# Optimization experiments

Measured on AMD Instinct MI355X. Metric: run time of the kernel, lower is better.

Reference implementation:

```python
import jax, jax.numpy as jnp
import numpy as np

TOPK, NUM_CLASSES, ALPHA, BETA, EPS = 13, 80, 1.0, 6.0, 1e-9
IOU_EPS = 1e-7  # eps used inside bbox_iou (ultralytics default)


def ciou(box1, box2):
    # box1, box2: broadcastable [..., 4] in xyxy format; returns CIoU [..., 1]
    b1x1, b1y1, b1x2, b1y2 = jnp.split(box1, 4, axis=-1)
    b2x1, b2y1, b2x2, b2y2 = jnp.split(box2, 4, axis=-1)
    w1, h1 = b1x2 - b1x1, b1y2 - b1y1 + IOU_EPS
    w2, h2 = b2x2 - b2x1, b2y2 - b2y1 + IOU_EPS
    inter = (jnp.clip(jnp.minimum(b1x2, b2x2) - jnp.maximum(b1x1, b2x1), 0.0) *
             jnp.clip(jnp.minimum(b1y2, b2y2) - jnp.maximum(b1y1, b2y1), 0.0))
    union = w1 * h1 + w2 * h2 - inter + IOU_EPS
    iou = inter / union
    cw = jnp.maximum(b1x2, b2x2) - jnp.minimum(b1x1, b2x1)  # enclosing box width
    ch = jnp.maximum(b1y2, b2y2) - jnp.minimum(b1y1, b2y1)
    c2 = cw ** 2 + ch ** 2 + IOU_EPS
    rho2 = ((b2x1 + b2x2 - b1x1 - b1x2) ** 2 + (b2y1 + b2y2 - b1y1 - b1y2) ** 2) / 4.0
    v = (4.0 / np.pi ** 2) * (jnp.arctan(w2 / h2) - jnp.arctan(w1 / h1)) ** 2
    alpha = jax.lax.stop_gradient(v / (v - iou + (1.0 + IOU_EPS)))  # torch: with no_grad
    return iou - (rho2 / c2 + v * alpha)


def tal_forward(pd_scores, pd_bboxes, anc_points, gt_labels, gt_bboxes, mask_gt):
    bs, na, nc = pd_scores.shape
    nb = gt_bboxes.shape[1]
    dt = pd_scores.dtype
    mgt = mask_gt[..., 0]  # (b, nb)

    # --- select_candidates_in_gts: anchor center strictly inside gt box ---
    lt, rb = gt_bboxes[..., :2], gt_bboxes[..., 2:]
    deltas = jnp.concatenate([anc_points[None, None, :, :] - lt[:, :, None, :],
                              rb[:, :, None, :] - anc_points[None, None, :, :]], axis=-1)  # (b,nb,na,4)
    mask_in_gts = (deltas.min(-1) > EPS).astype(dt)  # (b,nb,na)
    valid = (mask_in_gts * mgt[:, :, None]) > 0  # bool (b,nb,na)

    # --- get_box_metrics: class score gather + pairwise CIoU, masked ---
    lbl = gt_labels[..., 0].astype(jnp.int32)  # (b,nb)
    scores = jnp.take_along_axis(pd_scores, lbl[:, None, :], axis=2)  # (b,na,nb)
    bbox_scores = jnp.where(valid, scores.transpose(0, 2, 1), 0.0)  # (b,nb,na)
    ov = ciou(gt_bboxes[:, :, None, :], pd_bboxes[:, None, :, :])[..., 0]  # (b,nb,na)
    overlaps = jnp.where(valid, jnp.clip(ov, 0.0), 0.0)
    align_metric = bbox_scores ** ALPHA * overlaps ** BETA

    # --- select_topk_candidates ---
    _, tk_i = jax.lax.top_k(align_metric, TOPK)  # (b,nb,TOPK)
    tk_i = jnp.where(mgt[:, :, None] > 0, tk_i, 0)  # invalid gt rows -> all idx 0 (counted >1 -> zeroed)
    flat_i = tk_i.reshape(bs * nb, TOPK)
    cnt = jnp.zeros((bs * nb, na), jnp.int32).at[jnp.arange(bs * nb)[:, None], flat_i].add(1)
    cnt = cnt.reshape(bs, nb, na)
    is_in_topk = jnp.where(cnt > 1, 0, cnt).astype(dt)
    mask_pos = is_in_topk * mask_in_gts * mgt[:, :, None]

    # --- select_highest_overlaps: resolve anchors claimed by multiple gts ---
    fg = mask_pos.sum(-2)  # (b,na)
    mask_multi = fg[:, None, :] > 1
    max_idx = overlaps.argmax(1)  # (b,na)
    is_max = jax.nn.one_hot(max_idx, nb, dtype=dt).transpose(0, 2, 1)  # (b,nb,na)
    mask_pos = jnp.where(mask_multi, is_max, mask_pos)
    fg_mask = mask_pos.sum(-2)  # (b,na)
    target_gt_idx = mask_pos.argmax(-2)  # (b,na)

    # --- get_targets ---
    flat_gt_idx = target_gt_idx + jnp.arange(bs)[:, None] * nb  # (b,na)
    target_labels = jnp.clip(lbl.reshape(-1)[flat_gt_idx], 0)
    target_bboxes = gt_bboxes.reshape(-1, 4)[flat_gt_idx]  # (b,na,4)
    target_scores = jax.nn.one_hot(target_labels, nc, dtype=dt)
    target_scores = jnp.where(fg_mask[..., None] > 0, target_scores, 0.0)

    # --- normalization of align metric ---
    align_metric = align_metric * mask_pos
    pos_align = align_metric.max(-1, keepdims=True)  # (b,nb,1)
    pos_over = (overlaps * mask_pos).max(-1, keepdims=True)
    norm = (align_metric * pos_over / (pos_align + EPS)).max(-2)[..., None]  # (b,na,1)
    target_scores = target_scores * norm
    return target_labels, target_bboxes, target_scores, fg_mask > 0, target_gt_idx


def _make_boxes(key, shape):
    kc, kw = jax.random.split(key)
    c = jax.random.uniform(kc, shape[:-1] + (2,), jnp.float32, 60.0, 580.0)
    wh = jax.random.uniform(kw, shape[:-1] + (2,), jnp.float32, 20.0, 120.0)
    return jnp.concatenate([c - wh / 2, c + wh / 2], axis=-1)


def setup_inputs() -> dict:
    key = jax.random.key(0)
    ks = jax.random.split(key, 6)
    bs, na, nc, nb = 32, 8400, 80, 64
    pd_scores = jax.random.uniform(ks[0], (bs, na, nc), jnp.float32)
    pd_bboxes = _make_boxes(ks[1], (bs, na, 4))
    anc_points = jax.random.uniform(ks[2], (na, 2), jnp.float32, 0.0, 640.0)
    gt_labels = jax.random.randint(ks[3], (bs, nb, 1), 0, nc, dtype=jnp.int32)
    gt_bboxes = _make_boxes(ks[4], (bs, nb, 4))
    mask_gt = (jax.random.uniform(ks[5], (bs, nb, 1)) < 0.8).astype(jnp.float32)
    return {"pd_scores": pd_scores, "pd_bboxes": pd_bboxes, "anc_points": anc_points,
            "gt_labels": gt_labels, "gt_bboxes": gt_bboxes, "mask_gt": mask_gt}


def reference(pd_scores, pd_bboxes, anc_points, gt_labels, gt_bboxes, mask_gt):
    return tal_forward(pd_scores, pd_bboxes, anc_points, gt_labels, gt_bboxes, mask_gt)
```

## Files before the change

kernel.cpp:

```cpp
#include <hip/hip_runtime.h>
#include <stdint.h>

#pragma clang fp contract(off)

#define BS 32
#define NB 64
#define NA 8400
#define NC 80
#define TK 13
#define QMAX 1024
#define FORCED 32

__device__ __forceinline__ float ciou_f(float g0, float g1, float g2, float g3,
                                        float p0, float p1, float p2, float p3) {
    const float E = 1e-7f;
    float w1 = g2 - g0, h1 = (g3 - g1) + E;
    float w2 = p2 - p0, h2 = (p3 - p1) + E;
    float iw = fminf(g2, p2) - fmaxf(g0, p0); iw = fmaxf(iw, 0.f);
    float ih = fminf(g3, p3) - fmaxf(g1, p1); ih = fmaxf(ih, 0.f);
    float inter = iw * ih;
    float uni = w1 * h1 + w2 * h2 - inter + E;
    float iou = inter / uni;
    float cw = fmaxf(g2, p2) - fminf(g0, p0);
    float ch = fmaxf(g3, p3) - fminf(g1, p1);
    float c2 = cw * cw + ch * ch + E;
    float dx = p0 + p2 - g0 - g2;
    float dy = p1 + p3 - g1 - g3;
    float rho2 = (dx * dx + dy * dy) / 4.0f;
    float da = atanf(w2 / h2) - atanf(w1 / h1);
    float v = 0.4052847345693511f * (da * da);
    float alpha = v / ((v - iou) + 1.0000001f);
    return iou - (rho2 / c2 + v * alpha);
}

__global__ __launch_bounds__(256) void k1_topk(
    const float* __restrict__ pd_scores,
    const float* __restrict__ pd_bboxes,
    const float* __restrict__ anc,
    const int* __restrict__ gt_labels,
    const float* __restrict__ gt_bboxes,
    const float* __restrict__ mask_gt,
    int* __restrict__ tk_a, float* __restrict__ tk_v,
    float* __restrict__ tk_o, int* __restrict__ tk_f)
{
    int r = blockIdx.x;
    int b = r >> 6;
    int tid = threadIdx.x;

    if (mask_gt[r] <= 0.f) {
        if (tid < TK) {
            tk_a[r * TK + tid] = 0; tk_v[r * TK + tid] = 0.f;
            tk_o[r * TK + tid] = 0.f; tk_f[r * TK + tid] = 0;
        }
        return;
    }

    __shared__ int   qn;
    __shared__ int   qa[QMAX];
    __shared__ float qv[QMAX];
    __shared__ float qo[QMAX];

    float4 g = *(const float4*)&gt_bboxes[r * 4];
    int lbl = gt_labels[r];
    if (tid == 0) qn = 0;
    __syncthreads();

    for (int a = tid; a < NA; a += 256) {
        float2 ap = *(const float2*)&anc[2 * a];
        float d0 = ap.x - g.x, d1 = ap.y - g.y, d2 = g.z - ap.x, d3 = g.w - ap.y;
        float dmin = fminf(fminf(d0, d1), fminf(d2, d3));
        bool in = dmin > 1e-9f;
        if (in || a < FORCED) {
            int p = atomicAdd(&qn, 1);
            if (p < QMAX) qa[p] = a | (in ? (1 << 30) : 0);
        }
    }
    __syncthreads();
    int n = min(qn, QMAX);

    for (int c = tid; c < n; c += 256) {
        int packed = qa[c]; int a = packed & 0x3fffffff; bool in = (packed >> 30) & 1;
        float align = 0.f, ov = 0.f;
        if (in) {
            float4 p = *(const float4*)&pd_bboxes[(b * NA + a) * 4];
            ov = fmaxf(ciou_f(g.x, g.y, g.z, g.w, p.x, p.y, p.z, p.w), 0.f);
            float sc = pd_scores[(b * NA + a) * NC + lbl];
            float o2 = ov * ov;
            align = sc * (o2 * o2 * o2);
        }
        qv[c] = align; qo[c] = ov;
    }
    __syncthreads();

    if (tid < 64) {
        int lane = tid;
        unsigned consumed = 0;
        int wslot = 0; float wval = 0.f;
        for (int round = 0; round < TK; round++) {
            float bv = -2.f; int bgi = 0x7fffffff; int bsl = 0;
            int li = 0;
            for (int c = lane; c < n; c += 64, li++) {
                if (consumed & (1u << li)) continue;
                float v = qv[c]; int gi = qa[c] & 0x3fffffff;
                if (v > bv || (v == bv && gi < bgi)) { bv = v; bgi = gi; bsl = c; }
            }
            for (int off = 32; off; off >>= 1) {
                float v2 = __shfl_down(bv, off);
                int  gi2 = __shfl_down(bgi, off);
                int  sl2 = __shfl_down(bsl, off);
                if (v2 > bv || (v2 == bv && gi2 < bgi)) { bv = v2; bgi = gi2; bsl = sl2; }
            }
            int wsl = __shfl(bsl, 0);
            float wv = __shfl(bv, 0);
            if ((wsl & 63) == lane) consumed |= 1u << (wsl >> 6);
            if (lane == round) { wslot = wsl; wval = wv; }
        }
        if (lane < TK) {
            int packed = qa[wslot]; int a = packed & 0x3fffffff; int in = (packed >> 30) & 1;
            tk_a[r * TK + lane] = a;
            tk_v[r * TK + lane] = wval;
            tk_o[r * TK + lane] = qo[wslot];
            tk_f[r * TK + lane] = in;
        }
    }
}

__global__ void k2a_init(int* cnt, int* jA, unsigned* posA, unsigned* posO, int* mcount) {
    int i = blockIdx.x * 256 + threadIdx.x;
    if (i < BS * NA) { cnt[i] = 0; jA[i] = -1; }
    if (i < BS * NB) { posA[i] = 0u; posO[i] = 0u; }
    if (i == 0) *mcount = 0;
}

__global__ void k2b_count(const int* __restrict__ tk_a, const int* __restrict__ tk_f,
                          int* __restrict__ cnt) {
    int c = blockIdx.x * 256 + threadIdx.x;
    if (c >= BS * NB * TK) return;
    if (!tk_f[c]) return;
    int r = c / TK; int b = r >> 6;
    atomicAdd(&cnt[b * NA + tk_a[c]], 1);
}

__global__ void k2c_single(const int* __restrict__ tk_a, const float* __restrict__ tk_v,
                           const float* __restrict__ tk_o, const int* __restrict__ tk_f,
                           const int* __restrict__ cnt, int* __restrict__ jA,
                           float* __restrict__ av,
                           unsigned* __restrict__ posA, unsigned* __restrict__ posO,
                           int* __restrict__ mlist, int* __restrict__ mcount) {
    int c = blockIdx.x * 256 + threadIdx.x;
    if (c >= BS * NB * TK) return;
    if (!tk_f[c]) return;
    int r = c / TK; int b = r >> 6; int j = r & 63;
    int a = tk_a[c];
    int i = b * NA + a;
    if (cnt[i] == 1) {
        jA[i] = j; av[i] = tk_v[c];
        atomicMax(&posA[b * NB + j], __float_as_uint(tk_v[c]));
        atomicMax(&posO[b * NB + j], __float_as_uint(tk_o[c]));
    } else {
        int old = atomicCAS(&jA[i], -1, -2);
        if (old == -1) { int p = atomicAdd(mcount, 1); mlist[p] = i; }
    }
}

__global__ __launch_bounds__(256) void k2d_multi(
    const float* __restrict__ pd_scores,
    const float* __restrict__ pd_bboxes,
    const float* __restrict__ anc,
    const int* __restrict__ gt_labels,
    const float* __restrict__ gt_bboxes,
    const float* __restrict__ mask_gt,
    const int* __restrict__ mlist, const int* __restrict__ mcount,
    int* __restrict__ jA, float* __restrict__ av,
    unsigned* __restrict__ posA, unsigned* __restrict__ posO)
{
    int wid = (blockIdx.x * 256 + threadIdx.x) >> 6;
    int lane = threadIdx.x & 63;
    int nwaves = (gridDim.x * 256) >> 6;
    int nm = *mcount;
    for (int e = wid; e < nm; e += nwaves) {
        int i = mlist[e];
        int b = i / NA, a = i - b * NA;
        float2 ap = *(const float2*)&anc[2 * a];
        int row = b * NB + lane;
        float o = 0.f;
        if (mask_gt[row] > 0.f) {
            float4 g = *(const float4*)&gt_bboxes[row * 4];
            float d0 = ap.x - g.x, d1 = ap.y - g.y, d2 = g.z - ap.x, d3 = g.w - ap.y;
            float dmin = fminf(fminf(d0, d1), fminf(d2, d3));
            if (dmin > 1e-9f) {
                float4 p = *(const float4*)&pd_bboxes[(b * NA + a) * 4];
                o = fmaxf(ciou_f(g.x, g.y, g.z, g.w, p.x, p.y, p.z, p.w), 0.f);
            }
        }
        float bv = o; int bj = lane;
        for (int off = 32; off; off >>= 1) {
            float v2 = __shfl_down(bv, off);
            int  j2 = __shfl_down(bj, off);
            if (v2 > bv || (v2 == bv && j2 < bj)) { bv = v2; bj = j2; }
        }
        if (lane == 0) {
            int lbl = gt_labels[b * NB + bj];
            float sc = pd_scores[(b * NA + a) * NC + lbl];
            float o2 = bv * bv;
            float alg = sc * (o2 * o2 * o2);
            jA[i] = bj; av[i] = alg;
            atomicMax(&posA[b * NB + bj], __float_as_uint(alg));
            atomicMax(&posO[b * NB + bj], __float_as_uint(bv));
        }
    }
}

__global__ void k2f_final(const int* __restrict__ gt_labels,
                          const float* __restrict__ gt_bboxes,
                          const int* __restrict__ jA, const float* __restrict__ av,
                          const unsigned* __restrict__ posA, const unsigned* __restrict__ posO,
                          float* __restrict__ out,
                          float* __restrict__ normw, int* __restrict__ clsw) {
    int i = blockIdx.x * 256 + threadIdx.x;
    if (i >= BS * NA) return;
    int b = i / NA;
    int jj = jA[i];
    int tg = jj < 0 ? 0 : jj;
    int lab = gt_labels[b * NB + tg]; lab = lab < 0 ? 0 : lab;

    float* o_lab  = out;
    float* o_bbox = out + BS * NA;
    float* o_fg   = out + BS * NA * (5 + NC);
    float* o_idx  = o_fg + BS * NA;

    o_lab[i] = (float)lab;
    float4 bb = *(const float4*)&gt_bboxes[(b * NB + tg) * 4];
    *(float4*)&o_bbox[i * 4] = bb;
    o_fg[i] = (jj >= 0) ? 1.f : 0.f;
    o_idx[i] = (float)tg;

    float nrm = 0.f;
    if (jj >= 0) {
        float pa = __uint_as_float(posA[b * NB + jj]);
        float po = __uint_as_float(posO[b * NB + jj]);
        nrm = (av[i] * po) / (pa + 1e-9f);
    }
    normw[i] = nrm;
    clsw[i] = (jj >= 0) ? lab : -1;
}

__global__ void k3_scores(const float* __restrict__ normw, const int* __restrict__ clsw,
                          float* __restrict__ out) {
    int t = blockIdx.x * 256 + threadIdx.x;
    int row = t / 20;
    int c4 = (t - row * 20) * 4;
    int cls = clsw[row];
    float nv = normw[row];
    float4 v;
    v.x = (c4 + 0 == cls) ? nv : 0.f;
    v.y = (c4 + 1 == cls) ? nv : 0.f;
    v.z = (c4 + 2 == cls) ? nv : 0.f;
    v.w = (c4 + 3 == cls) ? nv : 0.f;
    float* o_sc = out + BS * NA * 5;
    *(float4*)&o_sc[row * NC + c4] = v;
}

extern "C" void kernel_launch(void* const* d_in, const int* in_sizes, int n_in,
                              void* d_out, int out_size, void* d_ws, size_t ws_size,
                              hipStream_t stream) {
    const float* pd_scores = (const float*)d_in[0];
    const float* pd_bboxes = (const float*)d_in[1];
    const float* anc       = (const float*)d_in[2];
    const int*   gt_labels = (const int*)d_in[3];
    const float* gt_bboxes = (const float*)d_in[4];
    const float* mask_gt   = (const float*)d_in[5];
    float* out = (float*)d_out;

    char* w = (char*)d_ws;
    const int NCAND = BS * NB * TK;
    int*      tk_a = (int*)w;      w += NCAND * 4;
    int*      tk_f = (int*)w;      w += NCAND * 4;
    float*    tk_v = (float*)w;    w += NCAND * 4;
    float*    tk_o = (float*)w;    w += NCAND * 4;
    int*      cnt  = (int*)w;      w += BS * NA * 4;
    int*      jA   = (int*)w;      w += BS * NA * 4;
    float*    av   = (float*)w;    w += BS * NA * 4;
    unsigned* posA = (unsigned*)w; w += BS * NB * 4;
    unsigned* posO = (unsigned*)w; w += BS * NB * 4;
    float*    normw = (float*)w;   w += BS * NA * 4;
    int*      clsw  = (int*)w;     w += BS * NA * 4;
    int*      mlist = (int*)w;     w += NCAND * 4;
    int*      mcount = (int*)w;    w += 4;

    k2a_init<<<(BS * NA + 255) / 256, 256, 0, stream>>>(cnt, jA, posA, posO, mcount);
    k1_topk<<<BS * NB, 256, 0, stream>>>(pd_scores, pd_bboxes, anc, gt_labels,
                                         gt_bboxes, mask_gt, tk_a, tk_v, tk_o, tk_f);
    k2b_count<<<(NCAND + 255) / 256, 256, 0, stream>>>(tk_a, tk_f, cnt);
    k2c_single<<<(NCAND + 255) / 256, 256, 0, stream>>>(tk_a, tk_v, tk_o, tk_f,
                                                        cnt, jA, av, posA, posO,
                                                        mlist, mcount);
    k2d_multi<<<52, 256, 0, stream>>>(pd_scores, pd_bboxes, anc, gt_labels,
                                      gt_bboxes, mask_gt, mlist, mcount,
                                      jA, av, posA, posO);
    k2f_final<<<(BS * NA + 255) / 256, 256, 0, stream>>>(gt_labels, gt_bboxes, jA, av,
                                                         posA, posO, out, normw, clsw);
    k3_scores<<<(BS * NA * NC / 4 + 255) / 256, 256, 0, stream>>>(normw, clsw, out);
}
```

Measured before the change: 223.5 us.

## Split candidate scan into separate anchor-parallel kernel and use single-wave top-k blocks

The in-box scan moves out of the per-GT top-k kernel into a new kernel where each thread takes one anchor, loops over the 64 GTs and appends matches to per-GT global lists through atomics. The top-k kernel then runs one 64-lane wave per GT, reads the precomputed list, adds the forced non-inside anchors with a ballot, and selects winners with less shared memory. The score output store becomes nontemporal. This adds one launch, global atomics and a workspace list capped at 640 entries per GT, and the order of list entries is no longer fixed, which only affects tie handling through anchor index.

```diff
diff --git a/kernel.cpp b/kernel.cpp
--- a/kernel.cpp
+++ b/kernel.cpp
@@ -8,8 +8,11 @@
 #define NA 8400
 #define NC 80
 #define TK 13
-#define QMAX 1024
+#define QCAP 640
+#define CMAX (QCAP + 32)
 #define FORCED 32
+
+typedef float floatx4 __attribute__((ext_vector_type(4)));
 
 __device__ __forceinline__ float ciou_f(float g0, float g1, float g2, float g3,
                                         float p0, float p1, float p2, float p3) {
@@ -33,102 +36,118 @@
     return iou - (rho2 / c2 + v * alpha);
 }
 
-__global__ __launch_bounds__(256) void k1_topk(
+__global__ __launch_bounds__(256) void k1a_scan(
+    const float* __restrict__ anc,
+    const float* __restrict__ gt_bboxes,
+    const float* __restrict__ mask_gt,
+    int* __restrict__ qcnt, int* __restrict__ qlist)
+{
+    int b = blockIdx.y;
+    int a = blockIdx.x * 256 + threadIdx.x;
+    if (a >= NA) return;
+    float2 ap = *(const float2*)&anc[2 * a];
+    for (int j = 0; j < NB; j++) {
+        int r = b * NB + j;
+        float mg = mask_gt[r];
+        float gx = gt_bboxes[r * 4 + 0], gy = gt_bboxes[r * 4 + 1];
+        float gz = gt_bboxes[r * 4 + 2], gw = gt_bboxes[r * 4 + 3];
+        float d0 = ap.x - gx, d1 = ap.y - gy, d2 = gz - ap.x, d3 = gw - ap.y;
+        float dmin = fminf(fminf(d0, d1), fminf(d2, d3));
+        if (mg > 0.f && dmin > 1e-9f) {
+            int p = atomicAdd(&qcnt[r], 1);
+            if (p < QCAP) qlist[r * QCAP + p] = a;
+        }
+    }
+}
+
+__global__ __launch_bounds__(64) void k1b_topk(
     const float* __restrict__ pd_scores,
     const float* __restrict__ pd_bboxes,
     const float* __restrict__ anc,
     const int* __restrict__ gt_labels,
     const float* __restrict__ gt_bboxes,
     const float* __restrict__ mask_gt,
+    const int* __restrict__ qcnt, const int* __restrict__ qlist,
     int* __restrict__ tk_a, float* __restrict__ tk_v,
     float* __restrict__ tk_o, int* __restrict__ tk_f)
 {
     int r = blockIdx.x;
     int b = r >> 6;
-    int tid = threadIdx.x;
+    int lane = threadIdx.x;
 
     if (mask_gt[r] <= 0.f) {
-        if (tid < TK) {
-            tk_a[r * TK + tid] = 0; tk_v[r * TK + tid] = 0.f;
-            tk_o[r * TK + tid] = 0.f; tk_f[r * TK + tid] = 0;
+        if (lane < TK) {
+            tk_a[r * TK + lane] = 0; tk_v[r * TK + lane] = 0.f;
+            tk_o[r * TK + lane] = 0.f; tk_f[r * TK + lane] = 0;
         }
         return;
     }
 
-    __shared__ int   qn;
-    __shared__ int   qa[QMAX];
-    __shared__ float qv[QMAX];
-    __shared__ float qo[QMAX];
+    __shared__ int   ca[CMAX];
+    __shared__ float cv[CMAX];
+    __shared__ float co[CMAX];
 
     float4 g = *(const float4*)&gt_bboxes[r * 4];
     int lbl = gt_labels[r];
-    if (tid == 0) qn = 0;
-    __syncthreads();
-
-    for (int a = tid; a < NA; a += 256) {
-        float2 ap = *(const float2*)&anc[2 * a];
+    int n0 = min(qcnt[r], QCAP);
+
+    bool add = false;
+    if (lane < FORCED) {
+        float2 ap = *(const float2*)&anc[2 * lane];
         float d0 = ap.x - g.x, d1 = ap.y - g.y, d2 = g.z - ap.x, d3 = g.w - ap.y;
         float dmin = fminf(fminf(d0, d1), fminf(d2, d3));
-        bool in = dmin > 1e-9f;
-        if (in || a < FORCED) {
-            int p = atomicAdd(&qn, 1);
-            if (p < QMAX) qa[p] = a | (in ? (1 << 30) : 0);
-        }
+        add = !(dmin > 1e-9f);
+    }
+    unsigned long long mb = __ballot(add);
+    int pos = __popcll(mb & ((1ull << lane) - 1ull));
+    if (add) { ca[n0 + pos] = lane; cv[n0 + pos] = 0.f; co[n0 + pos] = 0.f; }
+    int n = n0 + __popcll(mb);
+
+    for (int c = lane; c < n0; c += 64) {
+        int a = qlist[r * QCAP + c];
+        float4 p = *(const float4*)&pd_bboxes[(b * NA + a) * 4];
+        float ov = fmaxf(ciou_f(g.x, g.y, g.z, g.w, p.x, p.y, p.z, p.w), 0.f);
+        float sc = pd_scores[(b * NA + a) * NC + lbl];
+        float o2 = ov * ov;
+        ca[c] = a | (1 << 30); cv[c] = sc * (o2 * o2 * o2); co[c] = ov;
     }
     __syncthreads();
-    int n = min(qn, QMAX);
-
-    for (int c = tid; c < n; c += 256) {
-        int packed = qa[c]; int a = packed & 0x3fffffff; bool in = (packed >> 30) & 1;
-        float align = 0.f, ov = 0.f;
-        if (in) {
-            float4 p = *(const float4*)&pd_bboxes[(b * NA + a) * 4];
-            ov = fmaxf(ciou_f(g.x, g.y, g.z, g.w, p.x, p.y, p.z, p.w), 0.f);
-            float sc = pd_scores[(b * NA + a) * NC + lbl];
-            float o2 = ov * ov;
-            align = sc * (o2 * o2 * o2);
-        }
-        qv[c] = align; qo[c] = ov;
-    }
-    __syncthreads();
-
-    if (tid < 64) {
-        int lane = tid;
-        unsigned consumed = 0;
-        int wslot = 0; float wval = 0.f;
-        for (int round = 0; round < TK; round++) {
-            float bv = -2.f; int bgi = 0x7fffffff; int bsl = 0;
-            int li = 0;
-            for (int c = lane; c < n; c += 64, li++) {
-                if (consumed & (1u << li)) continue;
-                float v = qv[c]; int gi = qa[c] & 0x3fffffff;
-                if (v > bv || (v == bv && gi < bgi)) { bv = v; bgi = gi; bsl = c; }
-            }
-            for (int off = 32; off; off >>= 1) {
-                float v2 = __shfl_down(bv, off);
-                int  gi2 = __shfl_down(bgi, off);
-                int  sl2 = __shfl_down(bsl, off);
-                if (v2 > bv || (v2 == bv && gi2 < bgi)) { bv = v2; bgi = gi2; bsl = sl2; }
-            }
-            int wsl = __shfl(bsl, 0);
-            float wv = __shfl(bv, 0);
-            if ((wsl & 63) == lane) consumed |= 1u << (wsl >> 6);
-            if (lane == round) { wslot = wsl; wval = wv; }
-        }
-        if (lane < TK) {
-            int packed = qa[wslot]; int a = packed & 0x3fffffff; int in = (packed >> 30) & 1;
-            tk_a[r * TK + lane] = a;
-            tk_v[r * TK + lane] = wval;
-            tk_o[r * TK + lane] = qo[wslot];
-            tk_f[r * TK + lane] = in;
-        }
-    }
-}
-
-__global__ void k2a_init(int* cnt, int* jA, unsigned* posA, unsigned* posO, int* mcount) {
+
+    unsigned consumed = 0;
+    int wslot = 0; float wval = 0.f;
+    for (int round = 0; round < TK; round++) {
+        float bv = -2.f; int bgi = 0x7fffffff; int bsl = 0;
+        int li = 0;
+        for (int c = lane; c < n; c += 64, li++) {
+            if (consumed & (1u << li)) continue;
+            float v = cv[c]; int gi = ca[c] & 0x3fffffff;
+            if (v > bv || (v == bv && gi < bgi)) { bv = v; bgi = gi; bsl = c; }
+        }
+        for (int off = 32; off; off >>= 1) {
+            float v2 = __shfl_down(bv, off);
+            int  gi2 = __shfl_down(bgi, off);
+            int  sl2 = __shfl_down(bsl, off);
+            if (v2 > bv || (v2 == bv && gi2 < bgi)) { bv = v2; bgi = gi2; bsl = sl2; }
+        }
+        int wsl = __shfl(bsl, 0);
+        float wv = __shfl(bv, 0);
+        if ((wsl & 63) == lane) consumed |= 1u << (wsl >> 6);
+        if (lane == round) { wslot = wsl; wval = wv; }
+    }
+    if (lane < TK) {
+        int packed = ca[wslot]; int a = packed & 0x3fffffff; int in = (packed >> 30) & 1;
+        tk_a[r * TK + lane] = a;
+        tk_v[r * TK + lane] = wval;
+        tk_o[r * TK + lane] = co[wslot];
+        tk_f[r * TK + lane] = in;
+    }
+}
+
+__global__ void k2a_init(int* cnt, int* jA, unsigned* posA, unsigned* posO,
+                         int* mcount, int* qcnt) {
     int i = blockIdx.x * 256 + threadIdx.x;
     if (i < BS * NA) { cnt[i] = 0; jA[i] = -1; }
-    if (i < BS * NB) { posA[i] = 0u; posO[i] = 0u; }
+    if (i < BS * NB) { posA[i] = 0u; posO[i] = 0u; qcnt[i] = 0; }
     if (i == 0) *mcount = 0;
 }
 
@@ -252,13 +271,13 @@
     int c4 = (t - row * 20) * 4;
     int cls = clsw[row];
     float nv = normw[row];
-    float4 v;
+    floatx4 v;
     v.x = (c4 + 0 == cls) ? nv : 0.f;
     v.y = (c4 + 1 == cls) ? nv : 0.f;
     v.z = (c4 + 2 == cls) ? nv : 0.f;
     v.w = (c4 + 3 == cls) ? nv : 0.f;
     float* o_sc = out + BS * NA * 5;
-    *(float4*)&o_sc[row * NC + c4] = v;
+    __builtin_nontemporal_store(v, (floatx4*)&o_sc[row * NC + c4]);
 }
 
 extern "C" void kernel_launch(void* const* d_in, const int* in_sizes, int n_in,
@@ -286,11 +305,19 @@
     float*    normw = (float*)w;   w += BS * NA * 4;
     int*      clsw  = (int*)w;     w += BS * NA * 4;
     int*      mlist = (int*)w;     w += NCAND * 4;
-    int*      mcount = (int*)w;    w += 4;
-
-    k2a_init<<<(BS * NA + 255) / 256, 256, 0, stream>>>(cnt, jA, posA, posO, mcount);
-    k1_topk<<<BS * NB, 256, 0, stream>>>(pd_scores, pd_bboxes, anc, gt_labels,
-                                         gt_bboxes, mask_gt, tk_a, tk_v, tk_o, tk_f);
+    int*      mcount = (int*)w;    w += 64;
+    int*      qcnt  = (int*)w;     w += BS * NB * 4;
+    int*      qlist = (int*)w;     w += BS * NB * QCAP * 4;
+
+    k2a_init<<<(BS * NA + 255) / 256, 256, 0, stream>>>(cnt, jA, posA, posO,
+                                                        mcount, qcnt);
+    {
+        dim3 g((NA + 255) / 256, BS);
+        k1a_scan<<<g, 256, 0, stream>>>(anc, gt_bboxes, mask_gt, qcnt, qlist);
+    }
+    k1b_topk<<<BS * NB, 64, 0, stream>>>(pd_scores, pd_bboxes, anc, gt_labels,
+                                         gt_bboxes, mask_gt, qcnt, qlist,
+                                         tk_a, tk_v, tk_o, tk_f);
     k2b_count<<<(NCAND + 255) / 256, 256, 0, stream>>>(tk_a, tk_f, cnt);
     k2c_single<<<(NCAND + 255) / 256, 256, 0, stream>>>(tk_a, tk_v, tk_o, tk_f,
                                                         cnt, jA, av, posA, posO,
```

Result: slower. 253.0 us (+13.2%).
